# Kernel optimization log

Hardware: AMD Instinct MI355X
Metric: run time of the kernel (lower is better)

Reference implementation:

```python
import jax, jax.numpy as jnp
import numpy as np

SCALE = 1.0  # std of the Normal error model (init arg `scale`)
B, P, D, T = 32, 256, 64, 4096


def setup_inputs() -> dict:
    key = jax.random.key(0)
    k1, k2, k3 = jax.random.split(key, 3)
    data = jax.random.normal(k1, (B, P, D), dtype=jnp.float32)
    targets = jax.random.normal(k2, (B, P), dtype=jnp.float32)
    task_pool = jax.random.normal(k3, (T, D, 1), dtype=jnp.float32)
    return {"data": data, "targets": targets, "task_pool": task_pool}


def reference(data, targets, task_pool):
    # W: (n_dims, n_tasks), matching task_pool.squeeze(-1).T in the original
    W = task_pool[..., 0].T
    dt = data.dtype

    # Per-point, per-task predictions and Gaussian log-likelihoods, computed ONCE.
    # The original recomputes X@W and the log-prob sum for every prefix i (O(n^2));
    # here a single cumsum over the point axis reproduces the same prefix sums.
    pred_per_task = jnp.einsum('bpd,dt->bpt', data, W)          # (B, P, T)
    err = targets[..., None] - pred_per_task                     # (B, P, T)
    log_norm = -jnp.log(jnp.asarray(SCALE, dt)) - 0.5 * jnp.log(jnp.asarray(2.0 * np.pi, dt))
    scores = -0.5 * (err / SCALE) ** 2 + log_norm                # Normal(0, scale).log_prob

    cum = jnp.cumsum(scores, axis=1)                             # cum[:, i] = sum_{j<=i}
    # Posterior for predicting point i uses points 0..i-1; point 0 uses a uniform
    # posterior (original: W.mean(dim=1) == softmax(zeros) @ W.T).
    log_lik = jnp.concatenate([jnp.zeros_like(cum[:, :1]), cum[:, :-1]], axis=1)
    post = jax.nn.softmax(log_lik, axis=-1)                      # (B, P, T)

    w_mmse = jnp.einsum('bpt,dt->bpd', post, W)                  # posterior-mean weights
    return jnp.einsum('bpd,bpd->bp', data, w_mmse)               # (B, P)
```

## Files before the change

kernel.cpp:

```cpp
#include <hip/hip_runtime.h>
#include <hip/hip_bf16.h>
#include <math.h>

#define Bb 32
#define Pp 256
#define Dd 64
#define Tt 4096

typedef unsigned short ushort_t;
typedef __attribute__((ext_vector_type(8))) short bf16x8;
typedef __attribute__((ext_vector_type(4))) float f32x4;

#define TRIP_BYTES ((size_t)Bb * Pp * 64 * 16)
#define A_BF_BYTES ((size_t)Bb * Pp * Dd * 2)
#define B_BF_BYTES ((size_t)Tt * Dd * 2)
#define WS_NEED    (TRIP_BYTES + 2 * A_BF_BYTES + 2 * B_BF_BYTES)

#define MFMA6(a)                                                     \
  a = __builtin_amdgcn_mfma_f32_16x16x32_bf16(ah0, bh0, a, 0, 0, 0); \
  a = __builtin_amdgcn_mfma_f32_16x16x32_bf16(ah1, bh1, a, 0, 0, 0); \
  a = __builtin_amdgcn_mfma_f32_16x16x32_bf16(ah0, bl0, a, 0, 0, 0); \
  a = __builtin_amdgcn_mfma_f32_16x16x32_bf16(al0, bh0, a, 0, 0, 0); \
  a = __builtin_amdgcn_mfma_f32_16x16x32_bf16(ah1, bl1, a, 0, 0, 0); \
  a = __builtin_amdgcn_mfma_f32_16x16x32_bf16(al1, bh1, a, 0, 0, 0);

__global__ __launch_bounds__(256) void k_conv(const float* __restrict__ data,
                                              const float* __restrict__ Wt,
                                              ushort_t* __restrict__ Ah, ushort_t* __restrict__ Al,
                                              ushort_t* __restrict__ Bh, ushort_t* __restrict__ Bl) {
  const int i  = blockIdx.x * 256 + threadIdx.x;
  const int NA = Bb * Pp * Dd;
  const float x = (i < NA) ? data[i] : Wt[i - NA];
  const __hip_bfloat16 h = __float2bfloat16(x);
  const float hf = __bfloat162float(h);
  const __hip_bfloat16 l = __float2bfloat16(x - hf);
  if (i < NA) { Ah[i] = *(const ushort_t*)&h; Al[i] = *(const ushort_t*)&l; }
  else        { const int j = i - NA;
                Bh[j] = *(const ushort_t*)&h; Bl[j] = *(const ushort_t*)&l; }
}

__global__ __launch_bounds__(256, 2) void k_main(const ushort_t* __restrict__ Ah,
                                                 const ushort_t* __restrict__ Al,
                                                 const ushort_t* __restrict__ Bh,
                                                 const ushort_t* __restrict__ Bl,
                                                 const float* __restrict__ targets,
                                                 float4* __restrict__ triples) {
  __shared__ short Bhs[256 * 72];
  __shared__ short Bls[256 * 72];
  const int tid  = threadIdx.x;
  const int wid  = tid >> 6;
  const int lane = tid & 63;
  const int quad = lane >> 4;
  const int l16  = lane & 15;
  const int b     = blockIdx.x >> 4;
  const int strip = blockIdx.x & 15;
  const int t0    = strip * 256;

  {
    const float4* sh = (const float4*)(Bh + (size_t)t0 * Dd);
    const float4* sl = (const float4*)(Bl + (size_t)t0 * Dd);
#pragma unroll
    for (int j = 0; j < 8; ++j) {
      const int idx = tid + j * 256;
      const int tl  = idx >> 3;
      const int col = (idx & 7) * 8;
      *(float4*)&Bhs[tl * 72 + col] = sh[idx];
      *(float4*)&Bls[tl * 72 + col] = sl[idx];
    }
  }
  __syncthreads();

  const ushort_t* arow_base = Ah + (size_t)b * Pp * Dd;
  const ushort_t* alow_base = Al + (size_t)b * Pp * Dd;
  float4* __restrict__ trb  = triples + (size_t)b * Pp * 64;
  const int wstrip = strip * 4 + wid;

  float R[4];
#pragma unroll
  for (int nt = 0; nt < 4; ++nt) R[nt] = 0.f;

#pragma unroll 1
  for (int sg = 0; sg < 16; ++sg) {
    const int p0 = sg * 16;
    const size_t aoff = (size_t)(p0 + l16) * Dd + quad * 8;
    const bf16x8 ah0 = *(const bf16x8*)(arow_base + aoff);
    const bf16x8 ah1 = *(const bf16x8*)(arow_base + aoff + 32);
    const bf16x8 al0 = *(const bf16x8*)(alow_base + aoff);
    const bf16x8 al1 = *(const bf16x8*)(alow_base + aoff + 32);
    const float4 tq  = *(const float4*)(targets + b * Pp + p0 + quad * 4);

    float cc[4][4], av[4][4];
#pragma unroll
    for (int nt = 0; nt < 4; ++nt) {
      const int tl = wid * 64 + nt * 16 + l16;
      const int bo = tl * 72 + quad * 8;
      const bf16x8 bh0 = *(const bf16x8*)&Bhs[bo];
      const bf16x8 bh1 = *(const bf16x8*)&Bhs[bo + 32];
      const bf16x8 bl0 = *(const bf16x8*)&Bls[bo];
      const bf16x8 bl1 = *(const bf16x8*)&Bls[bo + 32];
      f32x4 a = (f32x4)0.f;
      MFMA6(a)

      float sc[4];
      { const float e = tq.x - a[0]; sc[0] = -0.5f * e * e; }
      { const float e = tq.y - a[1]; sc[1] = -0.5f * e * e; }
      { const float e = tq.z - a[2]; sc[2] = -0.5f * e * e; }
      { const float e = tq.w - a[3]; sc[3] = -0.5f * e * e; }

      const float colsum = (sc[0] + sc[1]) + (sc[2] + sc[3]);
      const float x1 = __shfl_xor(colsum, 16, 64);
      const float x2 = __shfl_xor(colsum, 32, 64);
      const float x3 = __shfl_xor(x1, 32, 64);
      const float pre = (quad == 0) ? 0.f
                      : (quad == 1) ? x1
                      : (quad == 2) ? (x2 + x3)
                                    : (x1 + x2 + x3);
      const float base = R[nt] + pre;
      cc[nt][0] = base;
      cc[nt][1] = base + sc[0];
      cc[nt][2] = cc[nt][1] + sc[1];
      cc[nt][3] = cc[nt][2] + sc[2];
#pragma unroll
      for (int r = 0; r < 4; ++r) av[nt][r] = a[r];

      R[nt] += ((colsum + x1) + (x2 + x3));
    }

    float mm[4], ss[4], vv[4];
#pragma unroll
    for (int r = 0; r < 4; ++r) {
      const float m01 = fmaxf(cc[0][r], cc[1][r]);
      const float m23 = fmaxf(cc[2][r], cc[3][r]);
      mm[r] = fmaxf(m01, m23);
      float s = 0.f, v = 0.f;
#pragma unroll
      for (int nt = 0; nt < 4; ++nt) {
        const float e = __expf(cc[nt][r] - mm[r]);
        s += e;
        v = fmaf(e, av[nt][r], v);
      }
      ss[r] = s; vv[r] = v;
    }

    float M[4];
#pragma unroll
    for (int r = 0; r < 4; ++r) M[r] = mm[r];
#pragma unroll
    for (int off = 1; off < 16; off <<= 1)
#pragma unroll
      for (int r = 0; r < 4; ++r) M[r] = fmaxf(M[r], __shfl_xor(M[r], off, 64));
#pragma unroll
    for (int r = 0; r < 4; ++r) {
      const float f = __expf(mm[r] - M[r]);
      ss[r] *= f; vv[r] *= f;
    }
#pragma unroll
    for (int off = 1; off < 16; off <<= 1)
#pragma unroll
      for (int r = 0; r < 4; ++r) {
        ss[r] += __shfl_xor(ss[r], off, 64);
        vv[r] += __shfl_xor(vv[r], off, 64);
      }

    if (l16 == 0) {
#pragma unroll
      for (int r = 0; r < 4; ++r) {
        const int p = p0 + quad * 4 + r;
        trb[p * 64 + wstrip] = make_float4(M[r], ss[r], vv[r], 0.f);
      }
    }
  }
}

__global__ __launch_bounds__(256) void k_merge(const float4* __restrict__ ws,
                                               float* __restrict__ out) {
  const int gt   = blockIdx.x * 256 + threadIdx.x;
  const int bp   = gt >> 6;
  const int lane = gt & 63;
  const float4 o = ws[(size_t)bp * 64 + lane];
  const float m = o.x, s = o.y, v = o.z;
  float M = m;
#pragma unroll
  for (int off = 32; off; off >>= 1) M = fmaxf(M, __shfl_xor(M, off, 64));
  const float f = __expf(m - M);
  float S = f * s, V = f * v;
#pragma unroll
  for (int off = 32; off; off >>= 1) {
    S += __shfl_xor(S, off, 64);
    V += __shfl_xor(V, off, 64);
  }
  if (lane == 0) out[bp] = V / S;
}

__global__ __launch_bounds__(256) void k_scan_fused(const float* __restrict__ data,
                                                    const float* __restrict__ targets,
                                                    const float* __restrict__ task_pool,
                                                    float4* __restrict__ ws) {
  const int b     = blockIdx.x >> 4;
  const int wid   = threadIdx.x >> 6;
  const int lane  = threadIdx.x & 63;
  const int chunk = ((blockIdx.x & 15) << 2) | wid;
  const int t     = (chunk << 6) | lane;
  float w[Dd];
#pragma unroll
  for (int d = 0; d < Dd; d += 4) {
    const float4 r = *(const float4*)(task_pool + (size_t)t * Dd + d);
    w[d] = r.x; w[d + 1] = r.y; w[d + 2] = r.z; w[d + 3] = r.w;
  }
  const float* drow = data + (size_t)b * (Pp * Dd);
  const float* tgt  = targets + b * Pp;
  float4* wsb       = ws + (size_t)b * (Pp * 64);
  float c = 0.f;
  for (int p = 0; p < Pp; ++p) {
    float a0 = 0.f, a1 = 0.f, a2 = 0.f, a3 = 0.f;
    const float* r = drow + p * Dd;
#pragma unroll
    for (int d = 0; d < Dd; d += 4) {
      a0 = fmaf(r[d], w[d], a0);         a1 = fmaf(r[d + 1], w[d + 1], a1);
      a2 = fmaf(r[d + 2], w[d + 2], a2); a3 = fmaf(r[d + 3], w[d + 3], a3);
    }
    const float pred = (a0 + a1) + (a2 + a3);
    float m = c;
#pragma unroll
    for (int off = 32; off; off >>= 1) m = fmaxf(m, __shfl_xor(m, off, 64));
    const float e = __expf(c - m);
    float s = e, v = e * pred;
#pragma unroll
    for (int off = 32; off; off >>= 1) {
      s += __shfl_xor(s, off, 64);
      v += __shfl_xor(v, off, 64);
    }
    if (lane == 0) wsb[p * 64 + chunk] = make_float4(m, s, v, 0.f);
    const float err = tgt[p] - pred;
    c = fmaf(-0.5f * err, err, c);
  }
}

extern "C" void kernel_launch(void* const* d_in, const int* in_sizes, int n_in,
                              void* d_out, int out_size, void* d_ws, size_t ws_size,
                              hipStream_t stream) {
  const float* data      = (const float*)d_in[0];
  const float* targets   = (const float*)d_in[1];
  const float* task_pool = (const float*)d_in[2];
  float* out = (float*)d_out;

  if (ws_size >= WS_NEED) {
    float4*   trips = (float4*)d_ws;
    char*     cb    = (char*)d_ws + TRIP_BYTES;
    ushort_t* Ah    = (ushort_t*)cb;
    ushort_t* Al    = (ushort_t*)(cb + A_BF_BYTES);
    ushort_t* Bh    = (ushort_t*)(cb + 2 * A_BF_BYTES);
    ushort_t* Bl    = (ushort_t*)(cb + 2 * A_BF_BYTES + B_BF_BYTES);
    k_conv <<<dim3((Bb * Pp * Dd + Tt * Dd) / 256), dim3(256), 0, stream>>>(
        data, task_pool, Ah, Al, Bh, Bl);
    k_main <<<dim3(Bb * 16), dim3(256), 0, stream>>>(Ah, Al, Bh, Bl, targets, trips);
    k_merge<<<dim3((Bb * Pp * 64) / 256), dim3(256), 0, stream>>>(trips, out);
  } else {
    float4* triples = (float4*)d_ws;
    k_scan_fused<<<dim3(512), dim3(256), 0, stream>>>(data, targets, task_pool, triples);
    k_merge<<<dim3((Bb * Pp * 64) / 256), dim3(256), 0, stream>>>(triples, out);
  }
}
```

Baseline: 104.9 us.

## Hold B operands in registers, prefetch A tiles, and use DPP reductions

Each wave loads its B (W) high and low bf16 fragments straight into registers, replacing the LDS staging and the block-wide barrier. The next A and target fragments are loaded one iteration ahead so global latency overlaps the MFMA and softmax work. The 16-lane max and sum reductions move from __shfl_xor to DPP quad_perm and row-mirror operations, which are cheaper lane exchanges. The trade-off is higher VGPR pressure, which could lower occupancy or cause spills.

```diff
diff --git a/kernel.cpp b/kernel.cpp
--- a/kernel.cpp
+++ b/kernel.cpp
@@ -16,13 +16,23 @@
 #define B_BF_BYTES ((size_t)Tt * Dd * 2)
 #define WS_NEED    (TRIP_BYTES + 2 * A_BF_BYTES + 2 * B_BF_BYTES)
 
-#define MFMA6(a)                                                     \
-  a = __builtin_amdgcn_mfma_f32_16x16x32_bf16(ah0, bh0, a, 0, 0, 0); \
-  a = __builtin_amdgcn_mfma_f32_16x16x32_bf16(ah1, bh1, a, 0, 0, 0); \
-  a = __builtin_amdgcn_mfma_f32_16x16x32_bf16(ah0, bl0, a, 0, 0, 0); \
-  a = __builtin_amdgcn_mfma_f32_16x16x32_bf16(al0, bh0, a, 0, 0, 0); \
-  a = __builtin_amdgcn_mfma_f32_16x16x32_bf16(ah1, bl1, a, 0, 0, 0); \
+template <int CTRL>
+__device__ __forceinline__ float dppf(float x) {
+  return __builtin_bit_cast(float,
+      __builtin_amdgcn_update_dpp(0, __builtin_bit_cast(int, x), CTRL, 0xF, 0xF, true));
+}
+
+__device__ __forceinline__ f32x4 mfma6(bf16x8 ah0, bf16x8 ah1, bf16x8 al0, bf16x8 al1,
+                                       bf16x8 bh0, bf16x8 bh1, bf16x8 bl0, bf16x8 bl1) {
+  f32x4 a = (f32x4)0.f;
+  a = __builtin_amdgcn_mfma_f32_16x16x32_bf16(ah0, bh0, a, 0, 0, 0);
+  a = __builtin_amdgcn_mfma_f32_16x16x32_bf16(ah1, bh1, a, 0, 0, 0);
+  a = __builtin_amdgcn_mfma_f32_16x16x32_bf16(ah0, bl0, a, 0, 0, 0);
+  a = __builtin_amdgcn_mfma_f32_16x16x32_bf16(al0, bh0, a, 0, 0, 0);
+  a = __builtin_amdgcn_mfma_f32_16x16x32_bf16(ah1, bl1, a, 0, 0, 0);
   a = __builtin_amdgcn_mfma_f32_16x16x32_bf16(al1, bh1, a, 0, 0, 0);
+  return a;
+}
 
 __global__ __launch_bounds__(256) void k_conv(const float* __restrict__ data,
                                               const float* __restrict__ Wt,
@@ -45,8 +55,6 @@
                                                  const ushort_t* __restrict__ Bl,
                                                  const float* __restrict__ targets,
                                                  float4* __restrict__ triples) {
-  __shared__ short Bhs[256 * 72];
-  __shared__ short Bls[256 * 72];
   const int tid  = threadIdx.x;
   const int wid  = tid >> 6;
   const int lane = tid & 63;
@@ -55,52 +63,48 @@
   const int b     = blockIdx.x >> 4;
   const int strip = blockIdx.x & 15;
   const int t0    = strip * 256;
-
-  {
-    const float4* sh = (const float4*)(Bh + (size_t)t0 * Dd);
-    const float4* sl = (const float4*)(Bl + (size_t)t0 * Dd);
-#pragma unroll
-    for (int j = 0; j < 8; ++j) {
-      const int idx = tid + j * 256;
-      const int tl  = idx >> 3;
-      const int col = (idx & 7) * 8;
-      *(float4*)&Bhs[tl * 72 + col] = sh[idx];
-      *(float4*)&Bls[tl * 72 + col] = sl[idx];
-    }
-  }
-  __syncthreads();
+  const int wstrip = strip * 4 + wid;
+
+  bf16x8 vbh0[4], vbh1[4], vbl0[4], vbl1[4];
+#pragma unroll
+  for (int nt = 0; nt < 4; ++nt) {
+    const size_t boff = (size_t)(t0 + wid * 64 + nt * 16 + l16) * Dd + quad * 8;
+    vbh0[nt] = *(const bf16x8*)(Bh + boff);
+    vbh1[nt] = *(const bf16x8*)(Bh + boff + 32);
+    vbl0[nt] = *(const bf16x8*)(Bl + boff);
+    vbl1[nt] = *(const bf16x8*)(Bl + boff + 32);
+  }
 
   const ushort_t* arow_base = Ah + (size_t)b * Pp * Dd;
   const ushort_t* alow_base = Al + (size_t)b * Pp * Dd;
   float4* __restrict__ trb  = triples + (size_t)b * Pp * 64;
-  const int wstrip = strip * 4 + wid;
 
   float R[4];
 #pragma unroll
   for (int nt = 0; nt < 4; ++nt) R[nt] = 0.f;
+
+  const size_t aoff0 = (size_t)l16 * Dd + quad * 8;
+  bf16x8 ah0 = *(const bf16x8*)(arow_base + aoff0);
+  bf16x8 ah1 = *(const bf16x8*)(arow_base + aoff0 + 32);
+  bf16x8 al0 = *(const bf16x8*)(alow_base + aoff0);
+  bf16x8 al1 = *(const bf16x8*)(alow_base + aoff0 + 32);
+  float4 tq  = *(const float4*)(targets + b * Pp + quad * 4);
 
 #pragma unroll 1
   for (int sg = 0; sg < 16; ++sg) {
-    const int p0 = sg * 16;
-    const size_t aoff = (size_t)(p0 + l16) * Dd + quad * 8;
-    const bf16x8 ah0 = *(const bf16x8*)(arow_base + aoff);
-    const bf16x8 ah1 = *(const bf16x8*)(arow_base + aoff + 32);
-    const bf16x8 al0 = *(const bf16x8*)(alow_base + aoff);
-    const bf16x8 al1 = *(const bf16x8*)(alow_base + aoff + 32);
-    const float4 tq  = *(const float4*)(targets + b * Pp + p0 + quad * 4);
+    const int pn = ((sg + 1) & 15) * 16;
+    const size_t an = (size_t)(pn + l16) * Dd + quad * 8;
+    const bf16x8 nah0 = *(const bf16x8*)(arow_base + an);
+    const bf16x8 nah1 = *(const bf16x8*)(arow_base + an + 32);
+    const bf16x8 nal0 = *(const bf16x8*)(alow_base + an);
+    const bf16x8 nal1 = *(const bf16x8*)(alow_base + an + 32);
+    const float4 ntq  = *(const float4*)(targets + b * Pp + pn + quad * 4);
 
     float cc[4][4], av[4][4];
 #pragma unroll
     for (int nt = 0; nt < 4; ++nt) {
-      const int tl = wid * 64 + nt * 16 + l16;
-      const int bo = tl * 72 + quad * 8;
-      const bf16x8 bh0 = *(const bf16x8*)&Bhs[bo];
-      const bf16x8 bh1 = *(const bf16x8*)&Bhs[bo + 32];
-      const bf16x8 bl0 = *(const bf16x8*)&Bls[bo];
-      const bf16x8 bl1 = *(const bf16x8*)&Bls[bo + 32];
-      f32x4 a = (f32x4)0.f;
-      MFMA6(a)
-
+      const f32x4 a = mfma6(ah0, ah1, al0, al1,
+                            vbh0[nt], vbh1[nt], vbl0[nt], vbl1[nt]);
       float sc[4];
       { const float e = tq.x - a[0]; sc[0] = -0.5f * e * e; }
       { const float e = tq.y - a[1]; sc[1] = -0.5f * e * e; }
@@ -146,29 +150,36 @@
 #pragma unroll
     for (int r = 0; r < 4; ++r) M[r] = mm[r];
 #pragma unroll
-    for (int off = 1; off < 16; off <<= 1)
-#pragma unroll
-      for (int r = 0; r < 4; ++r) M[r] = fmaxf(M[r], __shfl_xor(M[r], off, 64));
+    for (int r = 0; r < 4; ++r) M[r] = fmaxf(M[r], dppf<0xB1>(M[r]));
+#pragma unroll
+    for (int r = 0; r < 4; ++r) M[r] = fmaxf(M[r], dppf<0x4E>(M[r]));
+#pragma unroll
+    for (int r = 0; r < 4; ++r) M[r] = fmaxf(M[r], dppf<0x141>(M[r]));
+#pragma unroll
+    for (int r = 0; r < 4; ++r) M[r] = fmaxf(M[r], dppf<0x140>(M[r]));
 #pragma unroll
     for (int r = 0; r < 4; ++r) {
       const float f = __expf(mm[r] - M[r]);
       ss[r] *= f; vv[r] *= f;
     }
 #pragma unroll
-    for (int off = 1; off < 16; off <<= 1)
+    for (int r = 0; r < 4; ++r) { ss[r] += dppf<0xB1>(ss[r]);  vv[r] += dppf<0xB1>(vv[r]); }
+#pragma unroll
+    for (int r = 0; r < 4; ++r) { ss[r] += dppf<0x4E>(ss[r]);  vv[r] += dppf<0x4E>(vv[r]); }
+#pragma unroll
+    for (int r = 0; r < 4; ++r) { ss[r] += dppf<0x141>(ss[r]); vv[r] += dppf<0x141>(vv[r]); }
+#pragma unroll
+    for (int r = 0; r < 4; ++r) { ss[r] += dppf<0x140>(ss[r]); vv[r] += dppf<0x140>(vv[r]); }
+
+    if (l16 == 0) {
 #pragma unroll
       for (int r = 0; r < 4; ++r) {
-        ss[r] += __shfl_xor(ss[r], off, 64);
-        vv[r] += __shfl_xor(vv[r], off, 64);
-      }
-
-    if (l16 == 0) {
-#pragma unroll
-      for (int r = 0; r < 4; ++r) {
-        const int p = p0 + quad * 4 + r;
+        const int p = sg * 16 + quad * 4 + r;
         trb[p * 64 + wstrip] = make_float4(M[r], ss[r], vv[r], 0.f);
       }
     }
+
+    ah0 = nah0; ah1 = nah1; al0 = nal0; al1 = nal1; tq = ntq;
   }
 }
 
```

After: 101.0 us. -3.7%, faster.
